# Optimization experiments

Measured on AMD Instinct MI355X. Metric: run time of the kernel, lower is better.

The kernel has to match this reference:

```python
import jax, jax.numpy as jnp
import numpy as np

B, LT, LI, DT, DI, D, H = 128, 96, 64, 1024, 2048, 1024, 4
NEG = -2.0 ** 31  # tf.pow(-2.0, 31)
EPS = 1e-3        # keras LayerNormalization default epsilon


def _mha(q_in, k_in, v_in, q_mask, k_mask, Wq, Wk, Wv, Wo):
    # tf split-heads: chunk i of axis 2 -> head i; reshape (B,L,H,d) matches.
    d = D // H
    b = q_in.shape[0]
    q = (q_in @ Wq).reshape(b, -1, H, d)
    k = (k_in @ Wk).reshape(b, -1, H, d)
    v = (v_in @ Wv).reshape(b, -1, H, d)
    scores = jnp.einsum('bqhd,bkhd->bhqk', q, k) / jnp.sqrt(jnp.float32(d))
    mask = (q_mask != 0)[:, None, :, None] & (k_mask != 0)[:, None, None, :]  # [B,1,Lq,Lk]
    scores = jnp.where(mask, scores, NEG)
    attn = jax.nn.softmax(scores, axis=-1)
    attn = jnp.where(mask, attn, 0.0)  # dropout rate is 0.0 -> identity
    out = jnp.einsum('bhqk,bkhd->bqhd', attn, v).reshape(b, -1, D)
    return out @ Wo


def _ln(x, g, b):
    m = jnp.mean(x, axis=-1, keepdims=True)
    v = jnp.var(x, axis=-1, keepdims=True)
    return (x - m) / jnp.sqrt(v + EPS) * g + b


def setup_inputs() -> dict:
    key = jax.random.key(0)
    ks = iter(jax.random.split(key, 40))
    s = 0.02
    inp = {
        'text_embedding': jax.random.normal(next(ks), (B, LT, DT), jnp.float32),
        'image_embedding': jax.random.normal(next(ks), (B, LI, DI), jnp.float32),
        'text_mask': jax.random.randint(next(ks), (B, LT), 0, 2, jnp.int32),
        'image_mask': jax.random.randint(next(ks), (B, LI), 0, 2, jnp.int32),
        'W_tp': jax.random.normal(next(ks), (DT, D), jnp.float32) * s,
        'b_tp': jnp.zeros((D,), jnp.float32),
        'W_ip': jax.random.normal(next(ks), (DI, D), jnp.float32) * s,
        'b_ip': jnp.zeros((D,), jnp.float32),
        # text cross-attn (query=image_proj, key=text_proj, value=RAW text)
        'ta_Wq': jax.random.normal(next(ks), (D, D), jnp.float32) * s,
        'ta_Wk': jax.random.normal(next(ks), (D, D), jnp.float32) * s,
        'ta_Wv': jax.random.normal(next(ks), (DT, D), jnp.float32) * s,
        'ta_Wo': jax.random.normal(next(ks), (D, D), jnp.float32) * s,
        # image cross-attn (query=text_proj, key=image_proj, value=RAW image)
        'ia_Wq': jax.random.normal(next(ks), (D, D), jnp.float32) * s,
        'ia_Wk': jax.random.normal(next(ks), (D, D), jnp.float32) * s,
        'ia_Wv': jax.random.normal(next(ks), (DI, D), jnp.float32) * s,
        'ia_Wo': jax.random.normal(next(ks), (D, D), jnp.float32) * s,
        # self-attention blocks
        'ts_Wq': jax.random.normal(next(ks), (D, D), jnp.float32) * s,
        'ts_Wk': jax.random.normal(next(ks), (D, D), jnp.float32) * s,
        'ts_Wv': jax.random.normal(next(ks), (D, D), jnp.float32) * s,
        'ts_Wo': jax.random.normal(next(ks), (D, D), jnp.float32) * s,
        'is_Wq': jax.random.normal(next(ks), (D, D), jnp.float32) * s,
        'is_Wk': jax.random.normal(next(ks), (D, D), jnp.float32) * s,
        'is_Wv': jax.random.normal(next(ks), (D, D), jnp.float32) * s,
        'is_Wo': jax.random.normal(next(ks), (D, D), jnp.float32) * s,
        # layernorm params
        'ln_ta_g': jnp.ones((D,), jnp.float32), 'ln_ta_b': jnp.zeros((D,), jnp.float32),
        'ln_ia_g': jnp.ones((D,), jnp.float32), 'ln_ia_b': jnp.zeros((D,), jnp.float32),
        'ln_ts_g': jnp.ones((D,), jnp.float32), 'ln_ts_b': jnp.zeros((D,), jnp.float32),
        'ln_is_g': jnp.ones((D,), jnp.float32), 'ln_is_b': jnp.zeros((D,), jnp.float32),
    }
    return inp


def reference(text_embedding, image_embedding, text_mask, image_mask,
              W_tp, b_tp, W_ip, b_ip,
              ta_Wq, ta_Wk, ta_Wv, ta_Wo,
              ia_Wq, ia_Wk, ia_Wv, ia_Wo,
              ts_Wq, ts_Wk, ts_Wv, ts_Wo,
              is_Wq, is_Wk, is_Wv, is_Wo,
              ln_ta_g, ln_ta_b, ln_ia_g, ln_ia_b,
              ln_ts_g, ln_ts_b, ln_is_g, ln_is_b):
    text_proj = text_embedding @ W_tp + b_tp    # [B,LT,D]
    image_proj = image_embedding @ W_ip + b_ip  # [B,LI,D]
    # cross attention (note asymmetric query/key masks, raw-value inputs)
    text_att = _mha(image_proj, text_proj, text_embedding, image_mask, text_mask,
                    ta_Wq, ta_Wk, ta_Wv, ta_Wo)   # [B,LI,D]
    image_att = _mha(text_proj, image_proj, image_embedding, text_mask, image_mask,
                     ia_Wq, ia_Wk, ia_Wv, ia_Wo)  # [B,LT,D]
    text_att = _ln(text_att, ln_ta_g, ln_ta_b)
    image_att = _ln(image_att, ln_ia_g, ln_ia_b)
    # self attention
    text_att = _mha(text_att, text_att, text_att, image_mask, image_mask,
                    ts_Wq, ts_Wk, ts_Wv, ts_Wo)
    image_att = _mha(image_att, image_att, image_att, text_mask, text_mask,
                     is_Wq, is_Wk, is_Wv, is_Wo)
    text_att = _ln(text_att, ln_ts_g, ln_ts_b)
    image_att = _ln(image_att, ln_is_g, ln_is_b)
    return (text_att, image_att)
```

## Files before the change

kernel.cpp:

```cpp
#include <hip/hip_runtime.h>

typedef __bf16 bf16_t;
typedef __attribute__((ext_vector_type(8))) __bf16 bf16x8;
typedef __attribute__((ext_vector_type(4))) __bf16 bf16x4;
typedef __attribute__((ext_vector_type(4))) float f32x4;

__device__ __forceinline__ void async_copy16(const bf16_t* g, bf16_t* l) {
    __builtin_amdgcn_global_load_lds(
        (const __attribute__((address_space(1))) void*)g,
        (__attribute__((address_space(3))) void*)l, 16, 0, 0);
}

__global__ __launch_bounds__(256) void cvt_bf16(const float* __restrict__ in,
                                                bf16_t* __restrict__ out) {
    int i = (blockIdx.x * 256 + threadIdx.x) * 4;
    float4 v = *(const float4*)(in + i);
    bf16x4 o;
    o[0] = (__bf16)v.x; o[1] = (__bf16)v.y; o[2] = (__bf16)v.z; o[3] = (__bf16)v.w;
    *(bf16x4*)(out + i) = o;
}

__global__ __launch_bounds__(256) void transpose_group(const float* __restrict__ s0,
                                                       const float* __restrict__ s1,
                                                       const float* __restrict__ s2,
                                                       bf16_t* __restrict__ dst, int K) {
    const float* in;
    if (blockIdx.z == 0) in = s0;
    else if (blockIdx.z == 1) in = s1;
    else in = s2;
    bf16_t* out = dst + (size_t)blockIdx.z * 1024 * K;
    __shared__ float tile[32][33];
    int t = threadIdx.x;
    int tx = t & 31, ty = t >> 5;
    int n0 = blockIdx.x * 32, k0 = blockIdx.y * 32;
#pragma unroll
    for (int i = 0; i < 4; i++) {
        int k = k0 + ty + i * 8;
        tile[ty + i * 8][tx] = in[(size_t)k * 1024 + n0 + tx];
    }
    __syncthreads();
#pragma unroll
    for (int i = 0; i < 4; i++) {
        int n = n0 + ty + i * 8;
        out[(size_t)n * K + k0 + tx] = (bf16_t)tile[tx][ty + i * 8];
    }
}

__global__ __launch_bounds__(256) void fuse_bias(const float* __restrict__ src,
                                                 float* __restrict__ out) {
    int i = blockIdx.x * 256 + threadIdx.x;
    out[i] = (i < 1024) ? src[i] : 0.f;
}

__global__ __launch_bounds__(256) void gemm_bt(const bf16_t* __restrict__ A,
                                               const bf16_t* __restrict__ Bt,
                                               const float* __restrict__ bias,
                                               bf16_t* __restrict__ o0,
                                               bf16_t* __restrict__ o1,
                                               bf16_t* __restrict__ o2,
                                               int M, int N, int K) {
    __shared__ bf16_t As[128 * 32];
    __shared__ bf16_t Bs[128 * 32];
    const int t = threadIdx.x;
    const int w = t >> 6, lane = t & 63;
    const int quad = lane >> 4, l16 = lane & 15;
    const int bm = blockIdx.x * 128, bn = blockIdx.y * 128;
    const int wm = (w >> 1) * 64, wn = (w & 1) * 64;

    const f32x4 zero = {0.f, 0.f, 0.f, 0.f};
    f32x4 acc[4][4];
#pragma unroll
    for (int i = 0; i < 4; i++)
#pragma unroll
        for (int j = 0; j < 4; j++) acc[i][j] = zero;

    const int srow = t >> 2;
    const int scol = (t & 3) * 8;
    const bf16_t* ga = A + (size_t)(bm + srow) * K + scol;
    const bf16_t* gb = Bt + (size_t)(bn + srow) * K + scol;
    bf16_t* la = As + w * 512;
    bf16_t* lb = Bs + w * 512;

    for (int k0 = 0; k0 < K; k0 += 32) {
        async_copy16(ga + k0, la);
        async_copy16(ga + k0 + (size_t)64 * K, la + 2048);
        async_copy16(gb + k0, lb);
        async_copy16(gb + k0 + (size_t)64 * K, lb + 2048);
        __syncthreads();
        bf16x8 af[4], bf[4];
#pragma unroll
        for (int i = 0; i < 4; i++)
            af[i] = *(const bf16x8*)(As + (wm + i * 16 + l16) * 32 + quad * 8);
#pragma unroll
        for (int j = 0; j < 4; j++)
            bf[j] = *(const bf16x8*)(Bs + (wn + j * 16 + l16) * 32 + quad * 8);
#pragma unroll
        for (int i = 0; i < 4; i++)
#pragma unroll
            for (int j = 0; j < 4; j++)
                acc[i][j] = __builtin_amdgcn_mfma_f32_16x16x32_bf16(af[i], bf[j], acc[i][j], 0, 0, 0);
        __syncthreads();
    }

    bf16_t* out;
    if (bn < 1024) out = o0;
    else if (bn < 2048) out = o1;
    else out = o2;
    const int cb = bn & 1023;
    const int bbase = bn - cb;
#pragma unroll
    for (int i = 0; i < 4; i++) {
        int r0 = bm + wm + i * 16 + quad * 4;
#pragma unroll
        for (int j = 0; j < 4; j++) {
            int c = cb + wn + j * 16 + l16;
            float bsv = bias ? bias[bbase + c] : 0.f;
#pragma unroll
            for (int r = 0; r < 4; r++)
                out[(size_t)(r0 + r) * 1024 + c] = (bf16_t)(acc[i][j][r] + bsv);
        }
    }
}

template <int LQ, int LK>
__global__ __launch_bounds__(256) void attn_kernel(const bf16_t* __restrict__ Q,
                                                   const bf16_t* __restrict__ Kb,
                                                   const bf16_t* __restrict__ V,
                                                   const int* __restrict__ qmask,
                                                   const int* __restrict__ kmask,
                                                   bf16_t* __restrict__ O) {
    constexpr int VSTR = LK + 8;
    constexpr int NQT = LQ / 16, NKT = LK / 16, NKB = LK / 32;
    __shared__ bf16_t Vt[256 * VSTR];
    __shared__ bf16_t Pb[4 * 16 * LK];

    const int t = threadIdx.x;
    const int w = t >> 6, lane = t & 63;
    const int quad = lane >> 4, l16 = lane & 15;
    const int b = blockIdx.x >> 2;
    const int h = blockIdx.x & 3;
    const int hoff = h * 256;

    for (int idx = t; idx < LK * 32; idx += 256) {
        int k = idx % LK;
        int e0 = (idx / LK) * 8;
        bf16x8 v = *(const bf16x8*)(V + (size_t)(b * LK + k) * 1024 + hoff + e0);
#pragma unroll
        for (int j = 0; j < 8; j++) Vt[(e0 + j) * VSTR + k] = v[j];
    }
    __syncthreads();

    bf16_t* P = Pb + w * (16 * LK);

    for (int qt = w; qt < NQT; qt += 4) {
        const int qrow = b * LQ + qt * 16;
        bf16x8 qf[8];
#pragma unroll
        for (int kb = 0; kb < 8; kb++)
            qf[kb] = *(const bf16x8*)(Q + (size_t)(qrow + l16) * 1024 + hoff + kb * 32 + quad * 8);

        f32x4 s[NKT];
        const f32x4 zero = {0.f, 0.f, 0.f, 0.f};
#pragma unroll
        for (int nt = 0; nt < NKT; nt++) {
            f32x4 a = zero;
#pragma unroll
            for (int kb = 0; kb < 8; kb++) {
                bf16x8 kf = *(const bf16x8*)(Kb + (size_t)(b * LK + nt * 16 + l16) * 1024 + hoff + kb * 32 + quad * 8);
                a = __builtin_amdgcn_mfma_f32_16x16x32_bf16(qf[kb], kf, a, 0, 0, 0);
            }
            s[nt] = a;
        }

        int km[NKT];
#pragma unroll
        for (int nt = 0; nt < NKT; nt++) km[nt] = kmask[b * LK + nt * 16 + l16];
        int qmv[4];
#pragma unroll
        for (int r = 0; r < 4; r++) qmv[r] = qmask[b * LQ + qt * 16 + quad * 4 + r];

        float rmax[4], rsum[4];
#pragma unroll
        for (int r = 0; r < 4; r++) rmax[r] = -3.0e38f;
#pragma unroll
        for (int nt = 0; nt < NKT; nt++)
#pragma unroll
            for (int r = 0; r < 4; r++) {
                float v = s[nt][r] * 0.0625f;
                bool ok = (qmv[r] != 0) && (km[nt] != 0);
                s[nt][r] = ok ? v : -3.0e38f;
                rmax[r] = fmaxf(rmax[r], s[nt][r]);
            }
#pragma unroll
        for (int r = 0; r < 4; r++)
            for (int off = 1; off < 16; off <<= 1)
                rmax[r] = fmaxf(rmax[r], __shfl_xor(rmax[r], off, 16));
#pragma unroll
        for (int r = 0; r < 4; r++) rsum[r] = 0.f;
#pragma unroll
        for (int nt = 0; nt < NKT; nt++)
#pragma unroll
            for (int r = 0; r < 4; r++) {
                float p = (s[nt][r] > -1.0e38f) ? __expf(s[nt][r] - rmax[r]) : 0.f;
                s[nt][r] = p;
                rsum[r] += p;
            }
#pragma unroll
        for (int r = 0; r < 4; r++)
            for (int off = 1; off < 16; off <<= 1)
                rsum[r] += __shfl_xor(rsum[r], off, 16);
#pragma unroll
        for (int r = 0; r < 4; r++) rsum[r] = (rsum[r] > 0.f) ? 1.f / rsum[r] : 0.f;

#pragma unroll
        for (int nt = 0; nt < NKT; nt++)
#pragma unroll
            for (int r = 0; r < 4; r++)
                P[(quad * 4 + r) * LK + nt * 16 + l16] = (bf16_t)(s[nt][r] * rsum[r]);
        asm volatile("s_waitcnt lgkmcnt(0)" ::: "memory");

        bf16x8 pf[NKB];
#pragma unroll
        for (int kb = 0; kb < NKB; kb++)
            pf[kb] = *(const bf16x8*)(P + l16 * LK + kb * 32 + quad * 8);

#pragma unroll
        for (int et = 0; et < 16; et++) {
            f32x4 o = zero;
#pragma unroll
            for (int kb = 0; kb < NKB; kb++) {
                bf16x8 vf = *(const bf16x8*)(Vt + (et * 16 + l16) * VSTR + kb * 32 + quad * 8);
                o = __builtin_amdgcn_mfma_f32_16x16x32_bf16(pf[kb], vf, o, 0, 0, 0);
            }
#pragma unroll
            for (int r = 0; r < 4; r++)
                O[(size_t)(qrow + quad * 4 + r) * 1024 + hoff + et * 16 + l16] = (bf16_t)o[r];
        }
    }
}

__global__ __launch_bounds__(256) void ln_kernel(const bf16_t* __restrict__ in,
                                                 const float* __restrict__ g,
                                                 const float* __restrict__ be,
                                                 float* __restrict__ outF,
                                                 bf16_t* __restrict__ outB) {
    __shared__ float red[8];
    const int row = blockIdx.x, t = threadIdx.x;
    bf16x4 xb = *(const bf16x4*)(in + (size_t)row * 1024 + t * 4);
    float x0 = (float)xb[0], x1 = (float)xb[1], x2 = (float)xb[2], x3 = (float)xb[3];
    float s = x0 + x1 + x2 + x3;
    float ss = x0 * x0 + x1 * x1 + x2 * x2 + x3 * x3;
    for (int off = 1; off < 64; off <<= 1) {
        s += __shfl_xor(s, off);
        ss += __shfl_xor(ss, off);
    }
    int w = t >> 6, lane = t & 63;
    if (lane == 0) { red[w * 2] = s; red[w * 2 + 1] = ss; }
    __syncthreads();
    if (t == 0) {
        float a = 0.f, b2 = 0.f;
        for (int i = 0; i < 4; i++) { a += red[i * 2]; b2 += red[i * 2 + 1]; }
        red[0] = a; red[1] = b2;
    }
    __syncthreads();
    float mean = red[0] * (1.f / 1024.f);
    float var = red[1] * (1.f / 1024.f) - mean * mean;
    float rstd = rsqrtf(var + 1e-3f);
    float4 gv = *(const float4*)(g + t * 4);
    float4 bv = *(const float4*)(be + t * 4);
    float y0 = (x0 - mean) * rstd * gv.x + bv.x;
    float y1 = (x1 - mean) * rstd * gv.y + bv.y;
    float y2 = (x2 - mean) * rstd * gv.z + bv.z;
    float y3 = (x3 - mean) * rstd * gv.w + bv.w;
    if (outF) {
        float4 o = {y0, y1, y2, y3};
        *(float4*)(outF + (size_t)row * 1024 + t * 4) = o;
    }
    if (outB) {
        bf16x4 o;
        o[0] = (__bf16)y0; o[1] = (__bf16)y1; o[2] = (__bf16)y2; o[3] = (__bf16)y3;
        *(bf16x4*)(outB + (size_t)row * 1024 + t * 4) = o;
    }
}

extern "C" void kernel_launch(void* const* d_in, const int* in_sizes, int n_in,
                              void* d_out, int out_size, void* d_ws, size_t ws_size,
                              hipStream_t stream) {
    (void)in_sizes; (void)n_in; (void)out_size; (void)ws_size;
    const float* tE = (const float*)d_in[0];
    const float* iE = (const float*)d_in[1];
    const int* tMask = (const int*)d_in[2];
    const int* iMask = (const int*)d_in[3];

    const size_t MB = 1048576;
    char* ws = (char*)d_ws;
    bf16_t* WB = (bf16_t*)ws;
    float* biasT = (float*)(ws + 8 * MB);
    float* biasI = biasT + 2048;
    char* AB = ws + 9 * MB;
    auto buf = [&](int mb) { return (bf16_t*)(AB + (size_t)mb * MB); };

    auto TG = [&](int i0, int i1, int i2, int parts, int K) {
        transpose_group<<<dim3(32, K / 32, parts), 256, 0, stream>>>(
            (const float*)d_in[i0], i1 >= 0 ? (const float*)d_in[i1] : (const float*)d_in[i0],
            i2 >= 0 ? (const float*)d_in[i2] : (const float*)d_in[i0], WB, K);
    };
    auto gemm = [&](const bf16_t* A, const float* bias, bf16_t* out0, bf16_t* out1,
                    bf16_t* out2, int M, int N, int K) {
        gemm_bt<<<dim3(M / 128, N / 128), 256, 0, stream>>>(A, WB, bias, out0, out1, out2, M, N, K);
    };

    fuse_bias<<<8, 256, 0, stream>>>((const float*)d_in[5], biasT);
    fuse_bias<<<8, 256, 0, stream>>>((const float*)d_in[7], biasI);

    cvt_bf16<<<12288, 256, 0, stream>>>(tE, buf(88));
    TG(4, 10, -1, 2, 1024);
    gemm(buf(88), biasT, buf(32), buf(64), nullptr, 12288, 2048, 1024);
    cvt_bf16<<<16384, 256, 0, stream>>>(iE, buf(88));
    TG(6, 14, -1, 2, 2048);
    gemm(buf(88), biasI, buf(0), buf(16), nullptr, 8192, 2048, 2048);
    TG(9, 12, -1, 2, 1024);
    gemm(buf(32), nullptr, buf(88), buf(112), nullptr, 12288, 2048, 1024);
    TG(8, 13, -1, 2, 1024);
    gemm(buf(0), nullptr, buf(32), buf(48), nullptr, 8192, 2048, 1024);
    attn_kernel<64, 96><<<512, 256, 0, stream>>>(buf(32), buf(88), buf(64), iMask, tMask, buf(0));
    attn_kernel<96, 64><<<512, 256, 0, stream>>>(buf(112), buf(48), buf(16), tMask, iMask, buf(64));
    TG(11, -1, -1, 1, 1024);
    gemm(buf(0), nullptr, buf(32), nullptr, nullptr, 8192, 1024, 1024);
    ln_kernel<<<8192, 256, 0, stream>>>(buf(32), (const float*)d_in[24], (const float*)d_in[25], nullptr, buf(88));
    TG(15, -1, -1, 1, 1024);
    gemm(buf(64), nullptr, buf(0), nullptr, nullptr, 12288, 1024, 1024);
    ln_kernel<<<12288, 256, 0, stream>>>(buf(0), (const float*)d_in[26], (const float*)d_in[27], nullptr, buf(104));
    TG(16, 17, 18, 3, 1024);
    gemm(buf(88), nullptr, buf(0), buf(16), buf(32), 8192, 3072, 1024);
    attn_kernel<64, 64><<<512, 256, 0, stream>>>(buf(0), buf(16), buf(32), iMask, iMask, buf(48));
    TG(19, -1, -1, 1, 1024);
    gemm(buf(48), nullptr, buf(64), nullptr, nullptr, 8192, 1024, 1024);
    ln_kernel<<<8192, 256, 0, stream>>>(buf(64), (const float*)d_in[28], (const float*)d_in[29], (float*)d_out, nullptr);
    TG(20, 21, 22, 3, 1024);
    gemm(buf(104), nullptr, buf(0), buf(24), buf(48), 12288, 3072, 1024);
    attn_kernel<96, 96><<<512, 256, 0, stream>>>(buf(0), buf(24), buf(48), tMask, tMask, buf(72));
    TG(23, -1, -1, 1, 1024);
    gemm(buf(72), nullptr, buf(96), nullptr, nullptr, 12288, 1024, 1024);
    ln_kernel<<<12288, 256, 0, stream>>>(buf(96), (const float*)d_in[30], (const float*)d_in[31],
                                         (float*)d_out + 8388608, nullptr);
}
```

Baseline: 1.069 ms.

## Replace 128x128 GEMM with 256x256 4-stage pipelined swizzled GEMM

```diff
diff --git a/kernel.cpp b/kernel.cpp
--- a/kernel.cpp
+++ b/kernel.cpp
@@ -52,72 +52,145 @@
     out[i] = (i < 1024) ? src[i] : 0.f;
 }
 
-__global__ __launch_bounds__(256) void gemm_bt(const bf16_t* __restrict__ A,
-                                               const bf16_t* __restrict__ Bt,
-                                               const float* __restrict__ bias,
-                                               bf16_t* __restrict__ o0,
-                                               bf16_t* __restrict__ o1,
-                                               bf16_t* __restrict__ o2,
-                                               int M, int N, int K) {
-    __shared__ bf16_t As[128 * 32];
-    __shared__ bf16_t Bs[128 * 32];
+__global__ __launch_bounds__(512, 2) void gemm256(const bf16_t* __restrict__ A,
+                                                  const bf16_t* __restrict__ Bt,
+                                                  const float* __restrict__ bias,
+                                                  bf16_t* __restrict__ o0,
+                                                  bf16_t* __restrict__ o1,
+                                                  bf16_t* __restrict__ o2,
+                                                  int M, int N, int K) {
+    (void)M; (void)N;
+    __shared__ bf16_t Ls[65536];
     const int t = threadIdx.x;
     const int w = t >> 6, lane = t & 63;
-    const int quad = lane >> 4, l16 = lane & 15;
-    const int bm = blockIdx.x * 128, bn = blockIdx.y * 128;
-    const int wm = (w >> 1) * 64, wn = (w & 1) * 64;
+    const int l16 = lane & 15, quad = lane >> 4;
+    const int wm2 = w >> 2, wn4 = w & 3;
+
+    const int nx = gridDim.x;
+    const int nwg = nx * gridDim.y;
+    const int flat = blockIdx.y * nx + blockIdx.x;
+    const int chunk = nwg >> 3;
+    const int swz = (flat & 7) * chunk + (flat >> 3);
+    const int bm = (swz % nx) * 256;
+    const int bn = (swz / nx) * 256;
+
+    const int NT = K >> 5;
+
+    const int sl = t & 7;
+    const int pl = (t >> 3) & 63;
+    const int ss = sl ^ (pl & 7);
+    const int srow = (pl << 1) | (ss >> 2);
+    const int scol = (ss & 3) << 3;
+    const bf16_t* gA = A + (size_t)(bm + srow) * K + scol;
+    const bf16_t* gB = Bt + (size_t)(bn + srow) * K + scol;
+    const size_t rstep = (size_t)128 * K;
+    const int ldW = w * 512;
+
+    int offA[8], offB[4];
+#pragma unroll
+    for (int mf = 0; mf < 8; mf++) {
+        int row = wm2 * 128 + mf * 16 + l16;
+        int p = row >> 1;
+        int s2 = (((row & 1) << 2) | quad) ^ (p & 7);
+        offA[mf] = p * 64 + s2 * 8;
+    }
+#pragma unroll
+    for (int nf = 0; nf < 4; nf++) {
+        int row = wn4 * 64 + nf * 16 + l16;
+        int p = row >> 1;
+        int s2 = (((row & 1) << 2) | quad) ^ (p & 7);
+        offB[nf] = 8192 + p * 64 + s2 * 8;
+    }
 
     const f32x4 zero = {0.f, 0.f, 0.f, 0.f};
-    f32x4 acc[4][4];
-#pragma unroll
-    for (int i = 0; i < 4; i++)
+    f32x4 acc[8][4];
+#pragma unroll
+    for (int i = 0; i < 8; i++)
 #pragma unroll
         for (int j = 0; j < 4; j++) acc[i][j] = zero;
 
-    const int srow = t >> 2;
-    const int scol = (t & 3) * 8;
-    const bf16_t* ga = A + (size_t)(bm + srow) * K + scol;
-    const bf16_t* gb = Bt + (size_t)(bn + srow) * K + scol;
-    bf16_t* la = As + w * 512;
-    bf16_t* lb = Bs + w * 512;
-
-    for (int k0 = 0; k0 < K; k0 += 32) {
-        async_copy16(ga + k0, la);
-        async_copy16(ga + k0 + (size_t)64 * K, la + 2048);
-        async_copy16(gb + k0, lb);
-        async_copy16(gb + k0 + (size_t)64 * K, lb + 2048);
-        __syncthreads();
-        bf16x8 af[4], bf[4];
-#pragma unroll
-        for (int i = 0; i < 4; i++)
-            af[i] = *(const bf16x8*)(As + (wm + i * 16 + l16) * 32 + quad * 8);
-#pragma unroll
-        for (int j = 0; j < 4; j++)
-            bf[j] = *(const bf16x8*)(Bs + (wn + j * 16 + l16) * 32 + quad * 8);
-#pragma unroll
-        for (int i = 0; i < 4; i++)
-#pragma unroll
-            for (int j = 0; j < 4; j++)
-                acc[i][j] = __builtin_amdgcn_mfma_f32_16x16x32_bf16(af[i], bf[j], acc[i][j], 0, 0, 0);
-        __syncthreads();
-    }
-
-    bf16_t* out;
-    if (bn < 1024) out = o0;
-    else if (bn < 2048) out = o1;
-    else out = o2;
-    const int cb = bn & 1023;
-    const int bbase = bn - cb;
-#pragma unroll
-    for (int i = 0; i < 4; i++) {
-        int r0 = bm + wm + i * 16 + quad * 4;
-#pragma unroll
-        for (int j = 0; j < 4; j++) {
-            int c = cb + wn + j * 16 + l16;
-            float bsv = bias ? bias[bbase + c] : 0.f;
+#pragma unroll
+    for (int pt = 0; pt < 3; pt++) {
+        bf16_t* lb = Ls + pt * 16384 + ldW;
+        const bf16_t* a0 = gA + pt * 32;
+        const bf16_t* b0 = gB + pt * 32;
+        async_copy16(a0, lb);
+        async_copy16(a0 + rstep, lb + 4096);
+        async_copy16(b0, lb + 8192);
+        async_copy16(b0 + rstep, lb + 12288);
+    }
+    asm volatile("s_waitcnt vmcnt(8)" ::: "memory");
+    __builtin_amdgcn_s_barrier();
+    __builtin_amdgcn_sched_barrier(0);
+
+    for (int t0 = 0; t0 < NT; t0++) {
+        const bf16_t* cb = Ls + (t0 & 3) * 16384;
+        bf16_t* sb = Ls + ((t0 + 3) & 3) * 16384 + ldW;
+        const bf16_t* ga = gA + (size_t)(t0 + 3) * 32;
+        const bf16_t* gb = gB + (size_t)(t0 + 3) * 32;
+        const bool st = (t0 + 3 < NT);
+        bf16x8 bq[4], aq[4], ar[4];
+
+#pragma unroll
+        for (int nf = 0; nf < 4; nf++) bq[nf] = *(const bf16x8*)(cb + offB[nf]);
+#pragma unroll
+        for (int mf = 0; mf < 4; mf++) aq[mf] = *(const bf16x8*)(cb + offA[mf]);
+        if (st) {
+            async_copy16(ga, sb);
+            async_copy16(ga + rstep, sb + 4096);
+        }
+        __builtin_amdgcn_s_barrier();
+        __builtin_amdgcn_s_setprio(1);
+#pragma unroll
+        for (int mf = 0; mf < 4; mf++)
+#pragma unroll
+            for (int nf = 0; nf < 4; nf++)
+                acc[mf][nf] = __builtin_amdgcn_mfma_f32_16x16x32_bf16(aq[mf], bq[nf], acc[mf][nf], 0, 0, 0);
+        __builtin_amdgcn_s_setprio(0);
+        __builtin_amdgcn_s_barrier();
+
+#pragma unroll
+        for (int mf = 0; mf < 4; mf++) ar[mf] = *(const bf16x8*)(cb + offA[4 + mf]);
+        if (st) {
+            async_copy16(gb, sb + 8192);
+            async_copy16(gb + rstep, sb + 12288);
+        }
+        __builtin_amdgcn_s_barrier();
+        __builtin_amdgcn_s_setprio(1);
+#pragma unroll
+        for (int mf = 0; mf < 4; mf++)
+#pragma unroll
+            for (int nf = 0; nf < 4; nf++)
+                acc[4 + mf][nf] = __builtin_amdgcn_mfma_f32_16x16x32_bf16(ar[mf], bq[nf], acc[4 + mf][nf], 0, 0, 0);
+        __builtin_amdgcn_s_setprio(0);
+
+        if (t0 + 1 < NT) {
+            if (t0 + 3 < NT)      asm volatile("s_waitcnt vmcnt(8)" ::: "memory");
+            else if (t0 + 2 < NT) asm volatile("s_waitcnt vmcnt(4)" ::: "memory");
+            else                  asm volatile("s_waitcnt vmcnt(0)" ::: "memory");
+            __builtin_amdgcn_s_barrier();
+            __builtin_amdgcn_sched_barrier(0);
+        }
+    }
+
+    bf16_t* outp;
+    if (bn < 1024) outp = o0;
+    else if (bn < 2048) outp = o1;
+    else outp = o2;
+    const int cseg = bn & 1023;
+    float bsv[4];
+#pragma unroll
+    for (int nf = 0; nf < 4; nf++)
+        bsv[nf] = bias ? bias[bn + wn4 * 64 + nf * 16 + l16] : 0.f;
+#pragma unroll
+    for (int mf = 0; mf < 8; mf++) {
+        int r0 = bm + wm2 * 128 + mf * 16 + quad * 4;
+#pragma unroll
+        for (int nf = 0; nf < 4; nf++) {
+            int c = cseg + wn4 * 64 + nf * 16 + l16;
 #pragma unroll
             for (int r = 0; r < 4; r++)
-                out[(size_t)(r0 + r) * 1024 + c] = (bf16_t)(acc[i][j][r] + bsv);
+                outp[(size_t)(r0 + r) * 1024 + c] = (bf16_t)(acc[mf][nf][r] + bsv[nf]);
         }
     }
 }
@@ -307,7 +380,7 @@
     };
     auto gemm = [&](const bf16_t* A, const float* bias, bf16_t* out0, bf16_t* out1,
                     bf16_t* out2, int M, int N, int K) {
-        gemm_bt<<<dim3(M / 128, N / 128), 256, 0, stream>>>(A, WB, bias, out0, out1, out2, M, N, K);
+        gemm256<<<dim3(M / 256, N / 256), 512, 0, stream>>>(A, WB, bias, out0, out1, out2, M, N, K);
     };
 
     fuse_bias<<<8, 256, 0, stream>>>((const float*)d_in[5], biasT);
```

After: 998.3 us. 1.07x faster.
